# Kernel optimization log

Measured on AMD Instinct MI355X. Metric: run time of the kernel, lower is better.

Reference implementation:

```python
import jax, jax.numpy as jnp
import numpy as np

HEADS = 8
EPS = 1e-6

def _feature_map(x):
    return jax.nn.elu(x) + 1.0

def _linear_attention(q, k, v, motion_weight):
    # q,k,v: [..., N, dh]; motion_weight broadcastable to q or None
    q = _feature_map(q)
    k = _feature_map(k)
    if motion_weight is not None:
        q = q * motion_weight
    k_sum = k.sum(axis=-2, keepdims=True)                      # [...,1,dh]
    kv = jnp.einsum('...nd,...ne->...de', k, v)                # [...,dh,dh]
    out = jnp.einsum('...nd,...de->...ne', q, kv)              # [...,N,dh]
    z = 1.0 / (jnp.einsum('...nd,...md->...nm', q, k_sum) + EPS)  # [...,N,1]
    return out * z

def setup_inputs() -> dict:
    key = jax.random.key(0)
    k1, k2, k3, k4 = jax.random.split(key, 4)
    B, T, H, W, C = 2, 16, 48, 48, 512
    x = jax.random.normal(k1, (B, T, H, W, C), dtype=jnp.float32)
    motion_mag = jax.random.normal(k2, (B, T, H, W, 1), dtype=jnp.float32)
    W_qkv = jax.random.normal(k3, (C, 3 * C), dtype=jnp.float32) * 0.02
    temporal_emb = jax.random.normal(k4, (1, 1, 1, 1, C), dtype=jnp.float32)
    return {"x": x, "motion_mag": motion_mag, "W_qkv": W_qkv, "temporal_emb": temporal_emb}

def _split_heads(t, lead, n, heads, dh):
    # t: [lead, n, heads*dh] -> [lead, heads, n, dh]
    return t.reshape(lead, n, heads, dh).transpose(0, 2, 1, 3)

def reference(x, motion_mag, W_qkv, temporal_emb):
    B, T, H, W, C = x.shape
    dh = C // HEADS
    x = x + temporal_emb

    # ---- temporal linear attention over frame-averaged tokens ----
    x_time = x.reshape(B, T, H * W, C).mean(axis=2)            # [B,T,C]
    qkv = x_time @ W_qkv                                       # [B,T,3C]
    q, k, v = jnp.split(qkv, 3, axis=-1)
    q = _split_heads(q, B, T, HEADS, dh)                       # [B,h,T,dh]
    k = _split_heads(k, B, T, HEADS, dh)
    v = _split_heads(v, B, T, HEADS, dh)
    mm = motion_mag.reshape(B, T, -1).mean(axis=-1, keepdims=True)  # [B,T,1]
    mw_t = 1.0 + jnp.tanh(mm)[:, None]                         # [B,1,T,1]
    t_out = _linear_attention(q, k, v, mw_t)                   # [B,h,T,dh]
    t_out = t_out.transpose(0, 2, 1, 3).reshape(B, T, C)       # [B,T,C]

    # broadcast temporal output over spatial dims
    x_sp = x + t_out[:, :, None, None, :]                      # [B,T,H,W,C]

    # ---- global spatial linear attention per frame ----
    N = H * W
    x_flat = x_sp.reshape(B * T, N, C)
    qkv = x_flat @ W_qkv                                       # [BT,N,3C]
    q, k, v = jnp.split(qkv, 3, axis=-1)
    q = _split_heads(q, B * T, N, HEADS, dh)                   # [BT,h,N,dh]
    k = _split_heads(k, B * T, N, HEADS, dh)
    v = _split_heads(v, B * T, N, HEADS, dh)
    mm2 = motion_mag.reshape(B * T, N, 1)
    mw_s = 1.0 + jnp.tanh(mm2)[:, None]                        # [BT,1,N,1]
    s_out = _linear_attention(q, k, v, mw_s)                   # [BT,h,N,dh]
    s_out = s_out.transpose(0, 2, 1, 3).reshape(B, T, H, W, C)
    return s_out
```

## Files before the change

### kernel.cpp

```cpp
#include <hip/hip_runtime.h>
#include <cstddef>
#include <cstdint>

#define HEADS 8
#define DH 64
#define C 512
#define TC 1536
#define BT 32
#define NTOK 2304
#define TT 16
#define EPS 1e-6f

typedef __attribute__((ext_vector_type(8))) short bf16x8;
typedef __attribute__((ext_vector_type(4))) float f32x4;
typedef __attribute__((address_space(3))) void as3_void;
typedef __attribute__((address_space(1))) const void as1_cvoid;

#define SBAR() __builtin_amdgcn_s_barrier()
#define SCHED0() __builtin_amdgcn_sched_barrier(0)

__device__ __forceinline__ float fmap(float x) {
    return x > 0.f ? x + 1.f : __expf(x);
}
__device__ __forceinline__ unsigned short f2bf(float f) {
    unsigned int u = __float_as_uint(f);
    return (unsigned short)((u + 0x7fffu + ((u >> 16) & 1u)) >> 16);
}
__device__ __forceinline__ unsigned int pack2bf(float a, float b) {
    return (unsigned int)f2bf(a) | ((unsigned int)f2bf(b) << 16);
}
__device__ __forceinline__ float bf2f(unsigned short h) {
    return __uint_as_float(((unsigned int)h) << 16);
}
__device__ __forceinline__ void gload16(const void* g, void* l) {
    __builtin_amdgcn_global_load_lds((as1_cvoid*)(uintptr_t)g,
                                     (as3_void*)(uintptr_t)l, 16, 0, 0);
}

__global__ __launch_bounds__(256) void k_prep_w(
    const float* __restrict__ W, unsigned short* __restrict__ Wt) {
    __shared__ float tile[32][33];
    int col0 = blockIdx.x * 32, c0 = blockIdx.y * 32;
    int tx = threadIdx.x & 31, ty = threadIdx.x >> 5;
#pragma unroll
    for (int j = 0; j < 4; ++j) {
        int c = ty + j * 8;
        tile[c][tx] = W[(size_t)(c0 + c) * TC + col0 + tx];
    }
    __syncthreads();
#pragma unroll
    for (int j = 0; j < 4; ++j) {
        int col = ty + j * 8;
        Wt[(size_t)(col0 + col) * C + c0 + tx] = f2bf(tile[tx][col]);
    }
}

__global__ __launch_bounds__(256) void k_time_reduce(
    const float* __restrict__ x, const float* __restrict__ motion,
    float* __restrict__ xtraw, float* __restrict__ mmraw,
    unsigned short* __restrict__ xb) {
    int bt = blockIdx.x, sp = blockIdx.y, tid = threadIdx.x;
    int n0 = sp * 288, cid = tid * 2;
    const float* xp = x + ((size_t)(bt * NTOK + n0)) * C + cid;
    unsigned short* xbp = xb + ((size_t)(bt * NTOK + n0)) * C + cid;
    float s0 = 0.f, s1 = 0.f;
    for (int n = 0; n < 288; ++n) {
        float2 v = *(const float2*)(xp + (size_t)n * C);
        s0 += v.x;
        s1 += v.y;
        *(unsigned int*)(xbp + (size_t)n * C) = pack2bf(v.x, v.y);
    }
    atomicAdd(&xtraw[bt * C + cid], s0);
    atomicAdd(&xtraw[bt * C + cid + 1], s1);

    const float* mp = motion + (size_t)bt * NTOK + n0;
    float m = mp[tid];
    if (tid < 32) m += mp[256 + tid];
    __shared__ float red[256];
    red[tid] = m;
    __syncthreads();
    for (int s = 128; s > 0; s >>= 1) {
        if (tid < s) red[tid] += red[tid + s];
        __syncthreads();
    }
    if (tid == 0) atomicAdd(&mmraw[bt], red[0]);
}

__global__ __launch_bounds__(256) void k_time_qkv(
    const float* __restrict__ xtraw, const float* __restrict__ temb,
    const float* __restrict__ W, float* __restrict__ qkvt) {
    int bt = blockIdx.x, col = blockIdx.y * 256 + threadIdx.x, tid = threadIdx.x;
    __shared__ float xl[C];
    xl[tid]       = xtraw[bt * C + tid]       * (1.f / NTOK) + temb[tid];
    xl[tid + 256] = xtraw[bt * C + tid + 256] * (1.f / NTOK) + temb[tid + 256];
    __syncthreads();
    float a = 0.f;
#pragma unroll 8
    for (int c = 0; c < C; ++c) a += xl[c] * W[(size_t)c * TC + col];
    qkvt[(size_t)bt * TC + col] = a;
}

__global__ __launch_bounds__(256) void k_time_attn(
    const float* __restrict__ qkvt, const float* __restrict__ mmraw,
    const float* __restrict__ temb, float* __restrict__ bias) {
    int b = blockIdx.x, h = blockIdx.y, tid = threadIdx.x;
    int d = tid & 63, g = tid >> 6;
    __shared__ float qs[TT][DH], ks[TT][DH], vs[TT][DH], ksum[DH];
    __shared__ float kvl[DH][DH];
    for (int t = g; t < TT; t += 4) {
        size_t base = (size_t)(b * TT + t) * TC + h * DH + d;
        float mwt = 1.f + tanhf(mmraw[b * TT + t] * (1.f / NTOK));
        qs[t][d] = fmap(qkvt[base]) * mwt;
        ks[t][d] = fmap(qkvt[base + C]);
        vs[t][d] = qkvt[base + 2 * C];
    }
    __syncthreads();
    if (g == 0) {
        float s = 0.f;
        for (int t = 0; t < TT; ++t) s += ks[t][d];
        ksum[d] = s;
    }
    float kva[16];
#pragma unroll
    for (int i = 0; i < 16; ++i) kva[i] = 0.f;
    for (int t = 0; t < TT; ++t) {
        float kd = ks[t][d];
#pragma unroll
        for (int i = 0; i < 16; ++i) kva[i] += kd * vs[t][g * 16 + i];
    }
#pragma unroll
    for (int i = 0; i < 16; ++i) kvl[d][g * 16 + i] = kva[i];
    __syncthreads();
    for (int tt = 0; tt < 4; ++tt) {
        int t = g * 4 + tt;
        float acc = 0.f, zden = 0.f;
        for (int dd = 0; dd < DH; ++dd) {
            float qv = qs[t][dd];
            acc  += qv * kvl[dd][d];
            zden += qv * ksum[dd];
        }
        bias[(size_t)(b * TT + t) * C + h * DH + d] =
            acc / (zden + EPS) + temb[h * DH + d];
    }
}

__global__ __launch_bounds__(256) void k_bias_vec(
    const float* __restrict__ bias, const float* __restrict__ W,
    float* __restrict__ bvec) {
    int bt = blockIdx.x, col = blockIdx.y * 256 + threadIdx.x, tid = threadIdx.x;
    __shared__ float bl[C];
    bl[tid]       = bias[bt * C + tid];
    bl[tid + 256] = bias[bt * C + tid + 256];
    __syncthreads();
    float a = 0.f;
#pragma unroll 8
    for (int c = 0; c < C; ++c) a += bl[c] * W[(size_t)c * TC + col];
    bvec[(size_t)bt * TC + col] = a;
}

__global__ __launch_bounds__(512) void k_spatial_kv(
    const unsigned short* __restrict__ xb, const unsigned short* __restrict__ Wt,
    const float* __restrict__ bvec, float* __restrict__ kvw,
    float* __restrict__ ksw) {
    __shared__ __align__(16) char smem[115712];
    unsigned short* const Abuf[3] = {
        (unsigned short*)smem,
        (unsigned short*)(smem + 16384),
        (unsigned short*)(smem + 32768)};
    unsigned short* const Bbuf[2] = {
        (unsigned short*)(smem + 49152),
        (unsigned short*)(smem + 81920)};
    char* kvT = smem + 49152;
    float* bvl = (float*)(smem + 114688);

    const int s = blockIdx.x, hp = blockIdx.y, bt = blockIdx.z;
    const int tid = threadIdx.x, lane = tid & 63, w = tid >> 6;
    const int lm = lane & 15, quad = lane >> 4;
    const int mr = w & 1, nc = w >> 1;
    const int li8 = lane >> 3, lp = lane & 7;

    if (tid < 256) {
        int h2 = tid >> 7, j2 = tid & 127;
        int wr = (j2 < 64) ? (C + (hp * 2 + h2) * DH + j2)
                           : (2 * C + (hp * 2 + h2) * DH + (j2 - 64));
        bvl[tid] = bvec[(size_t)bt * TC + wr];
    }
    const unsigned short* srcA[2];
#pragma unroll
    for (int l = 0; l < 2; ++l) {
        int row = w * 16 + l * 8 + li8;
        int c = lp ^ (row & 7);
        srcA[l] = xb + ((size_t)(bt * NTOK + row)) * C + c * 8;
    }
    const unsigned short* srcB[4];
#pragma unroll
    for (int l = 0; l < 4; ++l) {
        int r = w * 32 + l * 8 + li8;
        int c = lp ^ (r & 7);
        int h2 = r >> 7, j2 = r & 127;
        int wr = (j2 < 64) ? (C + (hp * 2 + h2) * DH + j2)
                           : (2 * C + (hp * 2 + h2) * DH + (j2 - 64));
        srcB[l] = Wt + (size_t)wr * C + c * 8;
    }

    float ksp0 = 0.f, ksp1 = 0.f;
    f32x4 kvacc[2][2];
#pragma unroll
    for (int a = 0; a < 2; ++a)
#pragma unroll
        for (int b = 0; b < 2; ++b) kvacc[a][b] = (f32x4)0.f;

    auto STAGE_A = [&](unsigned short* As, int n0, int kc) {
#pragma unroll
        for (int l = 0; l < 2; ++l)
            gload16(srcA[l] + (size_t)n0 * C + kc * 64, As + (w * 16 + l * 8) * 64);
    };
    auto STAGE_B = [&](unsigned short* Bs, int kc) {
#pragma unroll
        for (int l = 0; l < 4; ++l)
            gload16(srcB[l] + kc * 64, Bs + (w * 32 + l * 8) * 64);
    };

#pragma unroll 1
    for (int t = 0; t < 3; ++t) {
        const int n0 = (s * 3 + t) * 128;
        f32x4 acc[4][4];
#pragma unroll
        for (int i = 0; i < 4; ++i)
#pragma unroll
            for (int j = 0; j < 4; ++j) acc[i][j] = (f32x4)0.f;

        STAGE_A(Abuf[0], n0, 0);
        STAGE_B(Bbuf[0], 0);
        SCHED0();
        STAGE_A(Abuf[1], n0, 1);
        SCHED0();
#pragma unroll
        for (int kc = 0; kc < 8; ++kc) {
            const unsigned short* As = Abuf[kc % 3];
            const unsigned short* Bs = Bbuf[kc & 1];
            if (kc < 7) {
                STAGE_B(Bbuf[(kc + 1) & 1], kc + 1);
                SCHED0();
            }
            if (kc < 6) {
                STAGE_A(Abuf[(kc + 2) % 3], n0, kc + 2);
                SCHED0();
            }
            if (kc < 6)
                asm volatile("s_waitcnt vmcnt(8)" ::: "memory");
            else if (kc == 6)
                asm volatile("s_waitcnt vmcnt(6)" ::: "memory");
            else
                asm volatile("s_waitcnt vmcnt(0)" ::: "memory");
            SBAR();
            SCHED0();
            __builtin_amdgcn_s_setprio(1);
#pragma unroll
            for (int ks = 0; ks < 2; ++ks) {
                bf16x8 af[4], bfr[4];
#pragma unroll
                for (int i = 0; i < 4; ++i) {
                    int row = mr * 64 + i * 16 + lm;
                    int p = (ks * 4 + quad) ^ (row & 7);
                    af[i] = *(const bf16x8*)&As[row * 64 + p * 8];
                }
#pragma unroll
                for (int j = 0; j < 4; ++j) {
                    int row = nc * 64 + j * 16 + lm;
                    int p = (ks * 4 + quad) ^ (row & 7);
                    bfr[j] = *(const bf16x8*)&Bs[row * 64 + p * 8];
                }
#pragma unroll
                for (int i = 0; i < 4; ++i)
#pragma unroll
                    for (int j = 0; j < 4; ++j)
                        acc[i][j] = __builtin_amdgcn_mfma_f32_16x16x32_bf16(
                            af[i], bfr[j], acc[i][j], 0, 0, 0);
            }
            __builtin_amdgcn_s_setprio(0);
            SCHED0();
            SBAR();
            SCHED0();
        }
#pragma unroll 1
        for (int ph = 0; ph < 2; ++ph) {
            __syncthreads();
            if ((nc >> 1) == ph) {
#pragma unroll
                for (int i = 0; i < 4; ++i) {
                    int tokb = mr * 64 + i * 16 + quad * 4;
                    int tc = tokb >> 3;
#pragma unroll
                    for (int j = 0; j < 4; ++j) {
                        int cg = nc * 64 + j * 16 + lm;
                        int cl = cg & 127;
                        float bv = bvl[cg];
                        f32x4 a4 = acc[i][j];
                        float v0 = a4[0] + bv, v1 = a4[1] + bv;
                        float v2 = a4[2] + bv, v3 = a4[3] + bv;
                        if (cl < 64) {
                            v0 = fmap(v0); v1 = fmap(v1);
                            v2 = fmap(v2); v3 = fmap(v3);
                        }
                        int p = (tc & 8) | ((tc & 7) ^ (cl & 7));
                        uint2 pk;
                        pk.x = pack2bf(v0, v1);
                        pk.y = pack2bf(v2, v3);
                        *(uint2*)(kvT + cl * 256 + p * 16 + (tokb & 7) * 2) = pk;
                    }
                }
            }
            __syncthreads();
            if (tid < 128) {
                int d = tid & 63, half = tid >> 6;
                float ssum = 0.f;
#pragma unroll
                for (int tc2 = 0; tc2 < 8; ++tc2) {
                    int tcc = half * 8 + tc2;
                    int p = (tcc & 8) | ((tcc & 7) ^ (d & 7));
                    bf16x8 v8 = *(const bf16x8*)(kvT + d * 256 + p * 16);
#pragma unroll
                    for (int q = 0; q < 8; ++q)
                        ssum += bf2f((unsigned short)v8[q]);
                }
                if (ph == 0) ksp0 += ssum; else ksp1 += ssum;
            }
#pragma unroll
            for (int dt2 = 0; dt2 < 2; ++dt2) {
                int drow = (mr * 2 + dt2) * 16 + lm;
                int erow = 64 + nc * 16 + lm;
#pragma unroll
                for (int ks2 = 0; ks2 < 4; ++ks2) {
                    int tcc = ks2 * 4 + quad;
                    int pA = (tcc & 8) | ((tcc & 7) ^ (drow & 7));
                    int pB = (tcc & 8) | ((tcc & 7) ^ (erow & 7));
                    bf16x8 ak = *(const bf16x8*)(kvT + drow * 256 + pA * 16);
                    bf16x8 bv8 = *(const bf16x8*)(kvT + erow * 256 + pB * 16);
                    kvacc[ph][dt2] = __builtin_amdgcn_mfma_f32_16x16x32_bf16(
                        ak, bv8, kvacc[ph][dt2], 0, 0, 0);
                }
            }
        }
        __syncthreads();
    }
#pragma unroll
    for (int ph = 0; ph < 2; ++ph) {
        float* kvp = kvw + (size_t)(bt * HEADS + hp * 2 + ph) * DH * DH;
#pragma unroll
        for (int dt2 = 0; dt2 < 2; ++dt2) {
            int d0 = (mr * 2 + dt2) * 16 + quad * 4;
            int e = nc * 16 + lm;
#pragma unroll
            for (int r = 0; r < 4; ++r)
                atomicAdd(&kvp[(d0 + r) * DH + e], kvacc[ph][dt2][r]);
        }
    }
    if (tid < 128) {
        int d = tid & 63;
        atomicAdd(&ksw[(bt * HEADS + hp * 2 + 0) * DH + d], ksp0);
        atomicAdd(&ksw[(bt * HEADS + hp * 2 + 1) * DH + d], ksp1);
    }
}

__global__ __launch_bounds__(256) void k_spatial_out(
    const unsigned short* __restrict__ xb, const unsigned short* __restrict__ Wt,
    const float* __restrict__ bvec, const float* __restrict__ motion,
    const float* __restrict__ kvw, const float* __restrict__ ksw,
    float* __restrict__ out) {
    __shared__ __align__(16) char smem[51712];
    unsigned short* A_s = (unsigned short*)smem;
    unsigned short* B_s = (unsigned short*)(smem + 16384);
    char* qs  = smem;
    char* kvT = smem + 32768;
    float* bvl = (float*)(smem + 49152);
    float* mwv = (float*)(smem + 49664);
    float* ksl = (float*)(smem + 50176);
    float* zv  = (float*)(smem + 50688);

    const int tile = blockIdx.x, hp = blockIdx.y, bt = blockIdx.z;
    const int tid = threadIdx.x, lane = tid & 63, w = tid >> 6;
    const int lm = lane & 15, quad = lane >> 4;
    const int mr = w & 1, nc = w >> 1;
    const int li8 = lane >> 3, lp = lane & 7;
    const int n0 = tile * 128;

    if (tid < 128) {
        bvl[tid] = bvec[(size_t)bt * TC + hp * 128 + tid];
        mwv[tid] = 1.f + tanhf(motion[(size_t)bt * NTOK + n0 + tid]);
        ksl[tid] = ksw[(bt * HEADS + hp * 2 + (tid >> 6)) * DH + (tid & 63)];
    }
    {
        int rr = tid & 127, hh = tid >> 7;
        int head = rr >> 6, e = rr & 63;
        const float* kvp = kvw + (size_t)(bt * HEADS + hp * 2 + head) * DH * DH;
#pragma unroll 8
        for (int d = hh * 32; d < hh * 32 + 32; ++d) {
            int p = (d >> 3) ^ (rr & 7);
            ((unsigned short*)(kvT + rr * 128 + p * 16))[d & 7] = f2bf(kvp[d * DH + e]);
        }
    }
    f32x4 acc[4][4];
#pragma unroll
    for (int i = 0; i < 4; ++i)
#pragma unroll
        for (int j = 0; j < 4; ++j) acc[i][j] = (f32x4)0.f;

    for (int kc = 0; kc < 8; ++kc) {
        __syncthreads();
#pragma unroll
        for (int l = 0; l < 4; ++l) {
            int rowbase = w * 32 + l * 8;
            int row = rowbase + li8;
            int c = lp ^ (row & 7);
            gload16(xb + ((size_t)(bt * NTOK + n0 + row)) * C + kc * 64 + c * 8,
                    A_s + rowbase * 64);
        }
#pragma unroll
        for (int l = 0; l < 4; ++l) {
            int rowbase = w * 32 + l * 8;
            int r = rowbase + li8;
            int c = lp ^ (r & 7);
            gload16(Wt + (size_t)(hp * 128 + r) * C + kc * 64 + c * 8,
                    B_s + rowbase * 64);
        }
        __syncthreads();
#pragma unroll
        for (int ks = 0; ks < 2; ++ks) {
            bf16x8 af[4], bfr[4];
#pragma unroll
            for (int i = 0; i < 4; ++i) {
                int row = mr * 64 + i * 16 + lm;
                int p = (ks * 4 + quad) ^ (row & 7);
                af[i] = *(const bf16x8*)&A_s[row * 64 + p * 8];
            }
#pragma unroll
            for (int j = 0; j < 4; ++j) {
                int row = nc * 64 + j * 16 + lm;
                int p = (ks * 4 + quad) ^ (row & 7);
                bfr[j] = *(const bf16x8*)&B_s[row * 64 + p * 8];
            }
#pragma unroll
            for (int i = 0; i < 4; ++i)
#pragma unroll
                for (int j = 0; j < 4; ++j)
                    acc[i][j] = __builtin_amdgcn_mfma_f32_16x16x32_bf16(
                        af[i], bfr[j], acc[i][j], 0, 0, 0);
        }
    }
    __syncthreads();
#pragma unroll
    for (int i = 0; i < 4; ++i) {
#pragma unroll
        for (int j = 0; j < 4; ++j) {
            int cl = nc * 64 + j * 16 + lm;
            float bv = bvl[cl];
            int cch = cl >> 3;
#pragma unroll
            for (int r = 0; r < 4; ++r) {
                int tok = mr * 64 + i * 16 + quad * 4 + r;
                float qv = fmap(acc[i][j][r] + bv) * mwv[tok];
                int p = (cch & 8) | ((cch & 7) ^ (tok & 7));
                ((unsigned short*)(qs + tok * 256 + p * 16))[cl & 7] = f2bf(qv);
            }
        }
    }
    __syncthreads();
    {
        int head = tid >> 7, tok = tid & 127;
        float zd = 0.f;
#pragma unroll
        for (int tc3 = 0; tc3 < 8; ++tc3) {
            int cch = head * 8 + tc3;
            int p = (cch & 8) | ((cch & 7) ^ (tok & 7));
            bf16x8 q8 = *(const bf16x8*)(qs + tok * 256 + p * 16);
#pragma unroll
            for (int q = 0; q < 8; ++q)
                zd += bf2f((unsigned short)q8[q]) * ksl[head * 64 + tc3 * 8 + q];
        }
        zv[head * 128 + tok] = 1.f / (zd + EPS);
    }
    __syncthreads();
    f32x4 oacc[4][4];
#pragma unroll
    for (int i = 0; i < 4; ++i)
#pragma unroll
        for (int j = 0; j < 4; ++j) oacc[i][j] = (f32x4)0.f;
#pragma unroll
    for (int ks3 = 0; ks3 < 2; ++ks3) {
        bf16x8 aq[4], bk[4];
#pragma unroll
        for (int i = 0; i < 4; ++i) {
            int tok = mr * 64 + i * 16 + lm;
            int cch = nc * 8 + ks3 * 4 + quad;
            int p = (cch & 8) | ((cch & 7) ^ (tok & 7));
            aq[i] = *(const bf16x8*)(qs + tok * 256 + p * 16);
        }
#pragma unroll
        for (int j = 0; j < 4; ++j) {
            int row = nc * 64 + j * 16 + lm;
            int tcc = ks3 * 4 + quad;
            int p = tcc ^ (row & 7);
            bk[j] = *(const bf16x8*)(kvT + row * 128 + p * 16);
        }
#pragma unroll
        for (int i = 0; i < 4; ++i)
#pragma unroll
            for (int j = 0; j < 4; ++j)
                oacc[i][j] = __builtin_amdgcn_mfma_f32_16x16x32_bf16(
                    aq[i], bk[j], oacc[i][j], 0, 0, 0);
    }
    const int h = hp * 2 + nc;
#pragma unroll
    for (int i = 0; i < 4; ++i)
#pragma unroll
        for (int r = 0; r < 4; ++r) {
            int tok = mr * 64 + i * 16 + quad * 4 + r;
            float z = zv[nc * 128 + tok];
#pragma unroll
            for (int j = 0; j < 4; ++j)
                out[((size_t)(bt * NTOK + n0 + tok)) * C + h * DH + j * 16 + lm] =
                    oacc[i][j][r] * z;
        }
}

extern "C" void kernel_launch(void* const* d_in, const int* in_sizes, int n_in,
                              void* d_out, int out_size, void* d_ws, size_t ws_size,
                              hipStream_t stream) {
    (void)in_sizes; (void)n_in; (void)out_size; (void)ws_size;
    const float* x      = (const float*)d_in[0];
    const float* motion = (const float*)d_in[1];
    const float* W      = (const float*)d_in[2];
    const float* temb   = (const float*)d_in[3];
    float* out = (float*)d_out;
    float* ws  = (float*)d_ws;

    float* kvw   = ws;
    float* ksw   = kvw + 1048576;
    float* xtraw = ksw + 16384;
    float* mmraw = xtraw + 16384;
    float* qkvt  = mmraw + 32;
    float* bias  = qkvt + 49152;
    float* bvec  = bias + 16384;
    unsigned short* Wt = (unsigned short*)(bvec + 49152);
    unsigned short* xb = (unsigned short*)(Wt + (size_t)TC * C);

    hipMemsetAsync(d_ws, 0,
                   (size_t)(1048576 + 16384 + 16384 + 32) * sizeof(float), stream);
    k_prep_w<<<dim3(48, 16), 256, 0, stream>>>(W, Wt);
    k_time_reduce<<<dim3(BT, 8), 256, 0, stream>>>(x, motion, xtraw, mmraw, xb);
    k_time_qkv<<<dim3(BT, 6), 256, 0, stream>>>(xtraw, temb, W, qkvt);
    k_time_attn<<<dim3(2, HEADS), 256, 0, stream>>>(qkvt, mmraw, temb, bias);
    k_bias_vec<<<dim3(BT, 6), 256, 0, stream>>>(bias, W, bvec);
    k_spatial_kv<<<dim3(6, 4, BT), 512, 0, stream>>>(xb, Wt, bvec, kvw, ksw);
    k_spatial_out<<<dim3(18, 4, BT), 256, 0, stream>>>(xb, Wt, bvec, motion,
                                                       kvw, ksw, out);
}
```

Measured before the change: 531.9 us.

## Double-buffer LDS staging in spatial output GEMM to overlap loads with MFMA

Splits the A/B shared-memory tiles of k_spatial_out into two ping-pong buffers and issues the global-to-LDS loads for the next K chunk before computing the current one. This lets memory latency overlap with MFMA work and removes one barrier per iteration. It also precomputes source pointers and fully unrolls the K loop. The cost is a larger LDS footprint (about 84 KB versus 52 KB per block), which may reduce how many blocks fit on a CU.

```diff
diff --git a/kernel.cpp b/kernel.cpp
--- a/kernel.cpp
+++ b/kernel.cpp
@@ -368,15 +368,19 @@
     const float* __restrict__ bvec, const float* __restrict__ motion,
     const float* __restrict__ kvw, const float* __restrict__ ksw,
     float* __restrict__ out) {
-    __shared__ __align__(16) char smem[51712];
-    unsigned short* A_s = (unsigned short*)smem;
-    unsigned short* B_s = (unsigned short*)(smem + 16384);
+    __shared__ __align__(16) char smem[84480];
+    unsigned short* const Abuf[2] = {
+        (unsigned short*)smem,
+        (unsigned short*)(smem + 32768)};
+    unsigned short* const Bbuf[2] = {
+        (unsigned short*)(smem + 16384),
+        (unsigned short*)(smem + 49152)};
     char* qs  = smem;
-    char* kvT = smem + 32768;
-    float* bvl = (float*)(smem + 49152);
-    float* mwv = (float*)(smem + 49664);
-    float* ksl = (float*)(smem + 50176);
-    float* zv  = (float*)(smem + 50688);
+    char* kvT = smem + 65536;
+    float* bvl = (float*)(smem + 81920);
+    float* mwv = (float*)(smem + 82432);
+    float* ksl = (float*)(smem + 82944);
+    float* zv  = (float*)(smem + 83456);
 
     const int tile = blockIdx.x, hp = blockIdx.y, bt = blockIdx.z;
     const int tid = threadIdx.x, lane = tid & 63, w = tid >> 6;
@@ -400,31 +404,45 @@
             ((unsigned short*)(kvT + rr * 128 + p * 16))[d & 7] = f2bf(kvp[d * DH + e]);
         }
     }
+    const unsigned short* srcA[4];
+#pragma unroll
+    for (int l = 0; l < 4; ++l) {
+        int row = w * 32 + l * 8 + li8;
+        int c = lp ^ (row & 7);
+        srcA[l] = xb + ((size_t)(bt * NTOK + n0 + row)) * C + c * 8;
+    }
+    const unsigned short* srcB[4];
+#pragma unroll
+    for (int l = 0; l < 4; ++l) {
+        int r = w * 32 + l * 8 + li8;
+        int c = lp ^ (r & 7);
+        srcB[l] = Wt + (size_t)(hp * 128 + r) * C + c * 8;
+    }
+    auto STAGE = [&](int buf, int kc) {
+#pragma unroll
+        for (int l = 0; l < 4; ++l)
+            gload16(srcA[l] + kc * 64, Abuf[buf] + (w * 32 + l * 8) * 64);
+#pragma unroll
+        for (int l = 0; l < 4; ++l)
+            gload16(srcB[l] + kc * 64, Bbuf[buf] + (w * 32 + l * 8) * 64);
+    };
+
     f32x4 acc[4][4];
 #pragma unroll
     for (int i = 0; i < 4; ++i)
 #pragma unroll
         for (int j = 0; j < 4; ++j) acc[i][j] = (f32x4)0.f;
 
+    STAGE(0, 0);
+    __syncthreads();
+#pragma unroll
     for (int kc = 0; kc < 8; ++kc) {
-        __syncthreads();
-#pragma unroll
-        for (int l = 0; l < 4; ++l) {
-            int rowbase = w * 32 + l * 8;
-            int row = rowbase + li8;
-            int c = lp ^ (row & 7);
-            gload16(xb + ((size_t)(bt * NTOK + n0 + row)) * C + kc * 64 + c * 8,
-                    A_s + rowbase * 64);
-        }
-#pragma unroll
-        for (int l = 0; l < 4; ++l) {
-            int rowbase = w * 32 + l * 8;
-            int r = rowbase + li8;
-            int c = lp ^ (r & 7);
-            gload16(Wt + (size_t)(hp * 128 + r) * C + kc * 64 + c * 8,
-                    B_s + rowbase * 64);
-        }
-        __syncthreads();
+        const unsigned short* As = Abuf[kc & 1];
+        const unsigned short* Bs = Bbuf[kc & 1];
+        if (kc < 7) {
+            STAGE((kc + 1) & 1, kc + 1);
+            SCHED0();
+        }
 #pragma unroll
         for (int ks = 0; ks < 2; ++ks) {
             bf16x8 af[4], bfr[4];
@@ -432,13 +450,13 @@
             for (int i = 0; i < 4; ++i) {
                 int row = mr * 64 + i * 16 + lm;
                 int p = (ks * 4 + quad) ^ (row & 7);
-                af[i] = *(const bf16x8*)&A_s[row * 64 + p * 8];
+                af[i] = *(const bf16x8*)&As[row * 64 + p * 8];
             }
 #pragma unroll
             for (int j = 0; j < 4; ++j) {
                 int row = nc * 64 + j * 16 + lm;
                 int p = (ks * 4 + quad) ^ (row & 7);
-                bfr[j] = *(const bf16x8*)&B_s[row * 64 + p * 8];
+                bfr[j] = *(const bf16x8*)&Bs[row * 64 + p * 8];
             }
 #pragma unroll
             for (int i = 0; i < 4; ++i)
@@ -447,8 +465,8 @@
                     acc[i][j] = __builtin_amdgcn_mfma_f32_16x16x32_bf16(
                         af[i], bfr[j], acc[i][j], 0, 0, 0);
         }
-    }
-    __syncthreads();
+        __syncthreads();
+    }
 #pragma unroll
     for (int i = 0; i < 4; ++i) {
 #pragma unroll
```

Measured after the change: 562.2 us. +5.7%, slower.
